# Performance work log

Measured on AMD Instinct MI355X. Metric: run time of the kernel, lower is better.

The kernel has to match this reference:

```python
import jax, jax.numpy as jnp
import numpy as np

V, B, F = 4, 8192, 128  # views, batch, fea_out
EPS = 1e-5  # torch BatchNorm1d default eps


def setup_inputs() -> dict:
    key = jax.random.key(0)
    k1, k2 = jax.random.split(key)
    x = jax.random.normal(k1, (V, B, F), dtype=jnp.float32)
    # Linear(F*F -> F) weight/bias; scale ~ kaiming-ish to keep activations sane
    W = jax.random.normal(k2, (F, F * F), dtype=jnp.float32) * 0.01
    b = jnp.zeros((F,), dtype=jnp.float32)
    gamma = jnp.ones((F,), dtype=jnp.float32)   # BN weight
    beta = jnp.zeros((F,), dtype=jnp.float32)   # BN bias
    return {"x": x, "W": W, "b": b, "gamma": gamma, "beta": beta}


def reference(x, W, b, gamma, beta):
    # x: [V, B, F] stack of views. Original loops over pairs (i<j):
    #   outer = x[i][:, :, None] @ x[j][:, None, :]          -> [B, F, F]
    #   flat  = outer.view(B, F*F)   (flat index = i*F + j)
    #   out   = ReLU(BN(Linear(flat)))
    # We fuse: Linear(flat(outer)) == einsum over W reshaped to [F_out, F, F],
    # avoiding the [B, F*F] intermediate. Same math.
    Vn, Bn, Fn = x.shape
    ii, jj = np.triu_indices(Vn, k=1)          # P = V*(V-1)/2 pairs
    x1 = x[ii]                                  # [P, B, F]
    x2 = x[jj]                                  # [P, B, F]
    Wr = W.reshape(Fn, Fn, Fn)                  # [F_out, F_i, F_j], matches row-major flatten
    # bilinear form per pair/batch: y[p,b,o] = sum_ij x1[p,b,i] * Wr[o,i,j] * x2[p,b,j] + b[o]
    y = jnp.einsum('pbi,oij,pbj->pbo', x1, Wr, x2) + b
    # BatchNorm1d in training mode: per-call batch stats (over batch axis, per pair),
    # biased variance, then affine, then ReLU.
    mean = jnp.mean(y, axis=1, keepdims=True)
    var = jnp.var(y, axis=1, keepdims=True)
    y_hat = (y - mean) * jax.lax.rsqrt(var + EPS)
    out = jax.nn.relu(gamma * y_hat + beta)     # [P, B, F]
    return out
```

## Files before the change

kernel.cpp:

```cpp
#include <hip/hip_runtime.h>

#define Fdim 128
#define Bsz  8192
#define Pn   6
#define EPSI 1e-5f

typedef _Float16 half8  __attribute__((ext_vector_type(8)));
typedef _Float16 half4t __attribute__((ext_vector_type(4)));
typedef float    float4t __attribute__((ext_vector_type(4)));

__constant__ int PAIR_A[6] = {0,0,0,1,1,2};
__constant__ int PAIR_B[6] = {1,2,3,2,3,3};

__global__ __launch_bounds__(256) void wprep(const float* __restrict__ W,
                                             _Float16* __restrict__ Wws) {
    int t  = blockIdx.x * 256 + threadIdx.x;
    int o  = t >> 11;
    int kg = t & 2047;
    int k0 = kg << 3;
    int c  = kg >> 2;
    int q  = kg & 3;
    int nt = o >> 4;
    int ol = o & 15;
    const float4t* src = (const float4t*)(W + (size_t)o * 16384 + k0);
    float4t a0 = src[0];
    float4t a1 = src[1];
    half8 h;
    h[0] = (_Float16)a0[0]; h[1] = (_Float16)a0[1];
    h[2] = (_Float16)a0[2]; h[3] = (_Float16)a0[3];
    h[4] = (_Float16)a1[0]; h[5] = (_Float16)a1[1];
    h[6] = (_Float16)a1[2]; h[7] = (_Float16)a1[3];
    *(half8*)(Wws + ((size_t)(c * 8 + nt) * 64 + q * 16 + ol) * 8) = h;
}

#define XPITCH 136

__global__ __launch_bounds__(256, 2) void gemm(const float* __restrict__ x,
                                               const _Float16* __restrict__ Wws,
                                               _Float16* __restrict__ yws,
                                               float* __restrict__ ssum,
                                               float* __restrict__ ssq) {
    __shared__ _Float16 x1t[128 * XPITCH];
    __shared__ _Float16 x2t[128 * XPITCH];

    int bid  = blockIdx.x;
    int p    = bid >> 7;
    int rem  = bid & 127;
    int mblk = rem >> 1;
    int nh   = rem & 1;
    int m0   = mblk * 128;
    int v1   = PAIR_A[p];
    int v2   = PAIR_B[p];
    int tid  = threadIdx.x;

    {
        const float4t* s1p = (const float4t*)(x + ((size_t)v1 * Bsz + m0) * Fdim);
        const float4t* s2p = (const float4t*)(x + ((size_t)v2 * Bsz + m0) * Fdim);
        for (int r = 0; r < 16; ++r) {
            int idx = r * 256 + tid;
            int row = idx >> 5;
            int col = (idx & 31) * 4;
            float4t a = s1p[idx];
            half4t h1; h1[0]=(_Float16)a[0]; h1[1]=(_Float16)a[1];
                       h1[2]=(_Float16)a[2]; h1[3]=(_Float16)a[3];
            *(half4t*)&x1t[row * XPITCH + col] = h1;
            float4t b = s2p[idx];
            half4t h2; h2[0]=(_Float16)b[0]; h2[1]=(_Float16)b[1];
                       h2[2]=(_Float16)b[2]; h2[3]=(_Float16)b[3];
            *(half4t*)&x2t[row * XPITCH + col] = h2;
        }
    }
    __syncthreads();

    int lane  = tid & 63;
    int w     = tid >> 6;
    int ol    = lane & 15;
    int q     = lane >> 4;
    int obase = nh * 64 + w * 16;
    int nt_g  = (nh << 2) + w;

    float4t acc[8];
#pragma unroll
    for (int mt = 0; mt < 8; ++mt) acc[mt] = (float4t){0.f, 0.f, 0.f, 0.f};

    const half8* wb = (const half8*)Wws;
    const size_t woff = (size_t)nt_g * 64 + lane;

    for (int jc = 0; jc < 4; ++jc) {
        half8 x2f[8];
#pragma unroll
        for (int mt = 0; mt < 8; ++mt)
            x2f[mt] = *(const half8*)&x2t[(mt * 16 + ol) * XPITCH + jc * 32 + q * 8];

        half8 bf0 = wb[(size_t)(0 * 4 + jc) * 512 + woff];
        half8 bf1 = wb[(size_t)(1 * 4 + jc) * 512 + woff];

        for (int i8 = 0; i8 < 16; ++i8) {
            half8 x1f[8];
#pragma unroll
            for (int mt = 0; mt < 8; ++mt)
                x1f[mt] = *(const half8*)&x1t[(mt * 16 + ol) * XPITCH + i8 * 8];
#pragma unroll
            for (int ii = 0; ii < 8; ++ii) {
                int i  = i8 * 8 + ii;
                int ip = (i < 126) ? (i + 2) : 127;
                half8 bn = wb[(size_t)(ip * 4 + jc) * 512 + woff];
#pragma unroll
                for (int mt = 0; mt < 8; ++mt) {
                    _Float16 sc = x1f[mt][ii];
                    half8 a = x2f[mt] * sc;
                    acc[mt] = __builtin_amdgcn_mfma_f32_16x16x32_f16(a, bf0, acc[mt], 0, 0, 0);
                }
                bf0 = bf1;
                bf1 = bn;
            }
        }
    }

    float sum0 = 0.f, sq0 = 0.f;
#pragma unroll
    for (int mt = 0; mt < 8; ++mt) {
#pragma unroll
        for (int r = 0; r < 4; ++r) {
            float v = acc[mt][r];
            sum0 += v;
            sq0  += v * v;
            size_t row = (size_t)p * Bsz + m0 + mt * 16 + q * 4 + r;
            yws[row * Fdim + obase + ol] = (_Float16)v;
        }
    }
    sum0 += __shfl_xor(sum0, 16, 64);   sum0 += __shfl_xor(sum0, 32, 64);
    sq0  += __shfl_xor(sq0, 16, 64);    sq0  += __shfl_xor(sq0, 32, 64);
    if (q == 0) {
        atomicAdd(&ssum[p * Fdim + obase + ol], sum0);
        atomicAdd(&ssq [p * Fdim + obase + ol], sq0);
    }
}

__global__ __launch_bounds__(256) void bnrelu(const _Float16* __restrict__ yws,
                                              const float* __restrict__ ssum,
                                              const float* __restrict__ ssq,
                                              const float* __restrict__ gamma,
                                              const float* __restrict__ beta,
                                              float* __restrict__ out) {
    __shared__ float gs[128], sh[128];
    size_t ebase = (size_t)blockIdx.x * 1024;
    int p = (int)(ebase >> 20);
    int t = threadIdx.x;
    if (t < 128) {
        float mean = ssum[p * Fdim + t] * (1.0f / 8192.0f);
        float var  = ssq [p * Fdim + t] * (1.0f / 8192.0f) - mean * mean;
        float g    = gamma[t] * rsqrtf(var + EPSI);
        gs[t] = g;
        sh[t] = beta[t] - g * mean;
    }
    __syncthreads();
    size_t e0 = ebase + (size_t)t * 4;
    int o0 = (int)(e0 & 127);
    half4t y = *(const half4t*)(yws + e0);
    float4t r;
#pragma unroll
    for (int l = 0; l < 4; ++l) {
        float v = fmaf(gs[o0 + l], (float)y[l], sh[o0 + l]);
        r[l] = v > 0.f ? v : 0.f;
    }
    *(float4t*)(out + e0) = r;
}

extern "C" void kernel_launch(void* const* d_in, const int* in_sizes, int n_in,
                              void* d_out, int out_size, void* d_ws, size_t ws_size,
                              hipStream_t stream) {
    const float* x     = (const float*)d_in[0];
    const float* W     = (const float*)d_in[1];
    const float* gamma = (const float*)d_in[3];
    const float* beta  = (const float*)d_in[4];
    float* out = (float*)d_out;

    char* ws = (char*)d_ws;
    _Float16* yws = (_Float16*)ws;
    _Float16* Wws = (_Float16*)(ws + 12582912);
    float*    ssum = (float*)(ws + 16777216);
    float*    ssq  = ssum + Pn * Fdim;

    (void)hipMemsetAsync(ssum, 0, 2 * Pn * Fdim * sizeof(float), stream);
    wprep<<<1024, 256, 0, stream>>>(W, Wws);
    gemm<<<768, 256, 0, stream>>>(x, Wws, yws, ssum, ssq);
    bnrelu<<<6144, 256, 0, stream>>>(yws, ssum, ssq, gamma, beta, out);
}
```

Before: 277.5 us.

## Retile GEMM to 64-row blocks covering all 128 outputs per block

```diff
diff --git a/kernel.cpp b/kernel.cpp
--- a/kernel.cpp
+++ b/kernel.cpp
@@ -4,6 +4,8 @@
 #define Bsz  8192
 #define Pn   6
 #define EPSI 1e-5f
+#define MROWS 64
+#define XPITCH 136
 
 typedef _Float16 half8  __attribute__((ext_vector_type(8)));
 typedef _Float16 half4t __attribute__((ext_vector_type(4)));
@@ -33,22 +35,18 @@
     *(half8*)(Wws + ((size_t)(c * 8 + nt) * 64 + q * 16 + ol) * 8) = h;
 }
 
-#define XPITCH 136
-
-__global__ __launch_bounds__(256, 2) void gemm(const float* __restrict__ x,
+__global__ __launch_bounds__(256, 4) void gemm(const float* __restrict__ x,
                                                const _Float16* __restrict__ Wws,
                                                _Float16* __restrict__ yws,
                                                float* __restrict__ ssum,
                                                float* __restrict__ ssq) {
-    __shared__ _Float16 x1t[128 * XPITCH];
-    __shared__ _Float16 x2t[128 * XPITCH];
+    __shared__ _Float16 x1t[MROWS * XPITCH];
+    __shared__ _Float16 x2t[MROWS * XPITCH];
 
     int bid  = blockIdx.x;
     int p    = bid >> 7;
-    int rem  = bid & 127;
-    int mblk = rem >> 1;
-    int nh   = rem & 1;
-    int m0   = mblk * 128;
+    int mblk = bid & 127;
+    int m0   = mblk * MROWS;
     int v1   = PAIR_A[p];
     int v2   = PAIR_B[p];
     int tid  = threadIdx.x;
@@ -56,7 +54,7 @@
     {
         const float4t* s1p = (const float4t*)(x + ((size_t)v1 * Bsz + m0) * Fdim);
         const float4t* s2p = (const float4t*)(x + ((size_t)v2 * Bsz + m0) * Fdim);
-        for (int r = 0; r < 16; ++r) {
+        for (int r = 0; r < 8; ++r) {
             int idx = r * 256 + tid;
             int row = idx >> 5;
             int col = (idx & 31) * 4;
@@ -76,64 +74,80 @@
     int w     = tid >> 6;
     int ol    = lane & 15;
     int q     = lane >> 4;
-    int obase = nh * 64 + w * 16;
-    int nt_g  = (nh << 2) + w;
-
-    float4t acc[8];
-#pragma unroll
-    for (int mt = 0; mt < 8; ++mt) acc[mt] = (float4t){0.f, 0.f, 0.f, 0.f};
+    int nt0   = w;
+    int nt1   = w + 4;
+
+    float4t acc[4][2];
+#pragma unroll
+    for (int mt = 0; mt < 4; ++mt) {
+        acc[mt][0] = (float4t){0.f, 0.f, 0.f, 0.f};
+        acc[mt][1] = (float4t){0.f, 0.f, 0.f, 0.f};
+    }
 
     const half8* wb = (const half8*)Wws;
-    const size_t woff = (size_t)nt_g * 64 + lane;
+    const size_t woff0 = (size_t)nt0 * 64 + lane;
+    const size_t woff1 = (size_t)nt1 * 64 + lane;
 
     for (int jc = 0; jc < 4; ++jc) {
-        half8 x2f[8];
-#pragma unroll
-        for (int mt = 0; mt < 8; ++mt)
+        half8 x2f[4];
+#pragma unroll
+        for (int mt = 0; mt < 4; ++mt)
             x2f[mt] = *(const half8*)&x2t[(mt * 16 + ol) * XPITCH + jc * 32 + q * 8];
 
-        half8 bf0 = wb[(size_t)(0 * 4 + jc) * 512 + woff];
-        half8 bf1 = wb[(size_t)(1 * 4 + jc) * 512 + woff];
+        half8 bfa0 = wb[(size_t)(0 * 4 + jc) * 512 + woff0];
+        half8 bfa1 = wb[(size_t)(0 * 4 + jc) * 512 + woff1];
+        half8 bfb0 = wb[(size_t)(1 * 4 + jc) * 512 + woff0];
+        half8 bfb1 = wb[(size_t)(1 * 4 + jc) * 512 + woff1];
 
         for (int i8 = 0; i8 < 16; ++i8) {
-            half8 x1f[8];
-#pragma unroll
-            for (int mt = 0; mt < 8; ++mt)
+            half8 x1f[4];
+#pragma unroll
+            for (int mt = 0; mt < 4; ++mt)
                 x1f[mt] = *(const half8*)&x1t[(mt * 16 + ol) * XPITCH + i8 * 8];
 #pragma unroll
             for (int ii = 0; ii < 8; ++ii) {
                 int i  = i8 * 8 + ii;
                 int ip = (i < 126) ? (i + 2) : 127;
-                half8 bn = wb[(size_t)(ip * 4 + jc) * 512 + woff];
-#pragma unroll
-                for (int mt = 0; mt < 8; ++mt) {
+                half8 bn0 = wb[(size_t)(ip * 4 + jc) * 512 + woff0];
+                half8 bn1 = wb[(size_t)(ip * 4 + jc) * 512 + woff1];
+#pragma unroll
+                for (int mt = 0; mt < 4; ++mt) {
                     _Float16 sc = x1f[mt][ii];
                     half8 a = x2f[mt] * sc;
-                    acc[mt] = __builtin_amdgcn_mfma_f32_16x16x32_f16(a, bf0, acc[mt], 0, 0, 0);
+                    acc[mt][0] = __builtin_amdgcn_mfma_f32_16x16x32_f16(a, bfa0, acc[mt][0], 0, 0, 0);
+                    acc[mt][1] = __builtin_amdgcn_mfma_f32_16x16x32_f16(a, bfa1, acc[mt][1], 0, 0, 0);
                 }
-                bf0 = bf1;
-                bf1 = bn;
+                bfa0 = bfb0; bfa1 = bfb1;
+                bfb0 = bn0;  bfb1 = bn1;
             }
         }
     }
 
-    float sum0 = 0.f, sq0 = 0.f;
-#pragma unroll
-    for (int mt = 0; mt < 8; ++mt) {
+    float sum0 = 0.f, sq0 = 0.f, sum1 = 0.f, sq1 = 0.f;
+    int col0 = nt0 * 16 + ol;
+    int col1 = nt1 * 16 + ol;
+#pragma unroll
+    for (int mt = 0; mt < 4; ++mt) {
 #pragma unroll
         for (int r = 0; r < 4; ++r) {
-            float v = acc[mt][r];
-            sum0 += v;
-            sq0  += v * v;
             size_t row = (size_t)p * Bsz + m0 + mt * 16 + q * 4 + r;
-            yws[row * Fdim + obase + ol] = (_Float16)v;
+            float v0 = acc[mt][0][r];
+            sum0 += v0; sq0 += v0 * v0;
+            yws[row * Fdim + col0] = (_Float16)v0;
+            float v1e = acc[mt][1][r];
+            sum1 += v1e; sq1 += v1e * v1e;
+            yws[row * Fdim + col1] = (_Float16)v1e;
         }
     }
-    sum0 += __shfl_xor(sum0, 16, 64);   sum0 += __shfl_xor(sum0, 32, 64);
-    sq0  += __shfl_xor(sq0, 16, 64);    sq0  += __shfl_xor(sq0, 32, 64);
+    sum0 += __shfl_xor(sum0, 16, 64);  sum0 += __shfl_xor(sum0, 32, 64);
+    sq0  += __shfl_xor(sq0, 16, 64);   sq0  += __shfl_xor(sq0, 32, 64);
+    sum1 += __shfl_xor(sum1, 16, 64);  sum1 += __shfl_xor(sum1, 32, 64);
+    sq1  += __shfl_xor(sq1, 16, 64);   sq1  += __shfl_xor(sq1, 32, 64);
     if (q == 0) {
-        atomicAdd(&ssum[p * Fdim + obase + ol], sum0);
-        atomicAdd(&ssq [p * Fdim + obase + ol], sq0);
+        atomicAdd(&ssum[p * Fdim + col0], sum0);
+        atomicAdd(&ssq [p * Fdim + col0], sq0);
+        atomicAdd(&ssum[p * Fdim + col1], sum1);
+        atomicAdd(&ssq [p * Fdim + col1], sq1);
     }
 }
 
```

New measurement: 596.3 us. +114.9%, slower.
